# Kernel optimization log

Measured on AMD Instinct MI355X. Metric: run time of the kernel, lower is better.

Reference implementation:

```python
import jax, jax.numpy as jnp
import numpy as np

B, CIN, COUT, K, SDIM, H, W = 16, 512, 512, 3, 512, 64, 64


def setup_inputs() -> dict:
    key = jax.random.key(0)
    k1, k2, k3, k4 = jax.random.split(key, 4)
    return {
        "x": jax.random.normal(k1, (B, CIN, H, W), dtype=jnp.float32),
        "style": jax.random.normal(k2, (B, SDIM), dtype=jnp.float32),
        "weight": jax.random.normal(k3, (COUT, CIN, K, K), dtype=jnp.float32),
        "style_w": jax.random.normal(k4, (CIN, SDIM), dtype=jnp.float32),
        "style_b": jnp.ones((CIN,), dtype=jnp.float32),  # bias.data.fill_(1.0)
    }


def reference(x, style, weight, style_w, style_b):
    batch, in_ch, h, w_size = x.shape
    out_ch, _, ks, _ = weight.shape
    pad = ks // 2
    # EqualizedLinear: runtime weight scaling by 1/sqrt(fan_in)
    lin_scale = 1.0 / np.sqrt(style_w.shape[1])
    s = style @ (style_w * lin_scale).T + style_b  # [B, Cin]
    # modulate
    conv_scale = 1.0 / np.sqrt(in_ch * ks * ks)
    wmod = (weight[None] * conv_scale) * s[:, None, :, None, None]  # [B,Cout,Cin,k,k]
    # demodulate
    dcoef = jax.lax.rsqrt(jnp.sum(jnp.square(wmod), axis=(2, 3, 4)) + 1e-8)  # [B,Cout]
    wmod = wmod * dcoef[:, :, None, None, None]
    # grouped conv with groups = batch
    x_r = x.reshape(1, batch * in_ch, h, w_size)
    w_r = wmod.reshape(batch * out_ch, in_ch, ks, ks)
    out = jax.lax.conv_general_dilated(
        x_r, w_r,
        window_strides=(1, 1),
        padding=[(pad, pad), (pad, pad)],
        dimension_numbers=("NCHW", "OIHW", "NCHW"),
        feature_group_count=batch,
    )
    return out.reshape(batch, out_ch, h, w_size)
```

## Files before the change

kernel.cpp:

```cpp
#include <hip/hip_runtime.h>
#include <math.h>

#define B 16
#define CIN 512
#define COUT 512
#define SDIM 512
#define H 64
#define W 64

typedef short s16x8 __attribute__((ext_vector_type(8)));
typedef float f32x4 __attribute__((ext_vector_type(4)));
typedef float f32x16 __attribute__((ext_vector_type(16)));

__device__ __constant__ float LIN_SCALE  = 0.04419417382415922f;
__device__ __constant__ float CONV_SCALE = 0.014731391274719742f;

__device__ __forceinline__ ushort f2bf(float f) {
  unsigned u = __float_as_uint(f);
  return (ushort)((u + 0x7FFFu + ((u >> 16) & 1u)) >> 16);
}

#define GLOAD16(g, l)                                           \
  __builtin_amdgcn_global_load_lds(                             \
      (const __attribute__((address_space(1))) unsigned*)(g),   \
      (__attribute__((address_space(3))) unsigned*)(l), 16, 0, 0)

__global__ __launch_bounds__(512) void style_mod_kernel(
    const float* __restrict__ style, const float* __restrict__ style_w,
    const float* __restrict__ style_b, float* __restrict__ s,
    float* __restrict__ s2) {
  const int b = blockIdx.x;
  const int ci = threadIdx.x;
  __shared__ float st[SDIM];
  st[ci] = style[b * SDIM + ci];
  __syncthreads();

  const float4* wr = reinterpret_cast<const float4*>(style_w + (size_t)ci * SDIM);
  float acc = 0.f;
#pragma unroll 4
  for (int k = 0; k < SDIM / 4; ++k) {
    float4 wv = wr[k];
    acc += st[4 * k + 0] * wv.x + st[4 * k + 1] * wv.y +
           st[4 * k + 2] * wv.z + st[4 * k + 3] * wv.w;
  }
  float v = acc * LIN_SCALE + style_b[ci];
  s[b * CIN + ci] = v;
  s2[b * CIN + ci] = v * v;
}

__global__ __launch_bounds__(256) void wsq_kernel(
    const float* __restrict__ weight, float* __restrict__ wsq) {
  const int i = blockIdx.x * blockDim.x + threadIdx.x;
  if (i >= COUT * CIN) return;
  const float* p = weight + (size_t)i * 9;
  float a = 0.f;
#pragma unroll
  for (int k = 0; k < 9; ++k) {
    float v = p[k];
    a += v * v;
  }
  wsq[i] = a;
}

__global__ __launch_bounds__(512) void dcoef_kernel(
    const float* __restrict__ s2, const float* __restrict__ wsq,
    float* __restrict__ outscale) {
  const int b = blockIdx.x;
  const int co = threadIdx.x;
  __shared__ float sh[CIN];
  sh[co] = s2[b * CIN + co];
  __syncthreads();

  const float4* wr = reinterpret_cast<const float4*>(wsq + (size_t)co * CIN);
  float acc = 0.f;
#pragma unroll 4
  for (int k = 0; k < CIN / 4; ++k) {
    float4 wv = wr[k];
    acc += sh[4 * k + 0] * wv.x + sh[4 * k + 1] * wv.y +
           sh[4 * k + 2] * wv.z + sh[4 * k + 3] * wv.w;
  }
  float d = rsqrtf(acc * CONV_SCALE * CONV_SCALE + 1e-8f);
  outscale[b * COUT + co] = d * CONV_SCALE;
}

__global__ __launch_bounds__(256) void pack_w_kernel(
    const float* __restrict__ w, ushort* __restrict__ wt) {
  const int t = blockIdx.x * 256 + threadIdx.x;
  const int s = t & 3;
  const int chunk = (t >> 2) & 15;
  const int co = t >> 6;
  const float4* wp =
      (const float4*)(w + ((size_t)co * 512 + chunk * 32 + s * 8) * 9);
  float wv[72];
#pragma unroll
  for (int i = 0; i < 18; ++i) {
    float4 v = wp[i];
    wv[4 * i + 0] = v.x; wv[4 * i + 1] = v.y;
    wv[4 * i + 2] = v.z; wv[4 * i + 3] = v.w;
  }
  const int sp = s ^ ((co >> 1) & 3);
  ushort* dst = wt + (size_t)chunk * 147456 + (size_t)co * 32 + sp * 8;
#pragma unroll
  for (int j = 0; j < 9; ++j) {
    s16x8 p;
#pragma unroll
    for (int i = 0; i < 8; ++i) p[i] = (short)f2bf(wv[i * 9 + j]);
    *(s16x8*)(dst + (size_t)j * 16384) = p;
  }
}

__global__ __launch_bounds__(256) void pack_x_kernel(
    const float* __restrict__ x, const float* __restrict__ smod,
    ushort* __restrict__ xp) {
  __shared__ float xt[32][65];
  __shared__ float sm[32];
  const int tid = threadIdx.x;
  const int gr = blockIdx.x, chunk = blockIdx.y, b = blockIdx.z;
  if (tid < 32) sm[tid] = smod[b * 512 + chunk * 32 + tid];
  {
    const int ci = tid >> 3, cq = tid & 7;
    const float4* rp = (const float4*)(
        x + (((size_t)b * 512 + chunk * 32 + ci) * 64 + gr) * 64 + cq * 8);
    float4 a = rp[0], c2 = rp[1];
    float* row = &xt[ci][cq * 8];
    row[0] = a.x; row[1] = a.y; row[2] = a.z; row[3] = a.w;
    row[4] = c2.x; row[5] = c2.y; row[6] = c2.z; row[7] = c2.w;
  }
  __syncthreads();
  const int c = tid >> 2, s = tid & 3;
  s16x8 p;
#pragma unroll
  for (int i = 0; i < 8; ++i)
    p[i] = (short)f2bf(xt[s * 8 + i][c] * sm[s * 8 + i]);
  const int sp = s ^ (((c + 1) >> 1) & 3);
  *(s16x8*)(xp + ((size_t)(b * 16 + chunk) * 64 + gr) * 2048 + c * 32 + sp * 8) = p;
}

#define XS4OFF 36864
#define DLDS4 79104

__global__ __launch_bounds__(256, 2) void conv_mfma5_kernel(
    const ushort* __restrict__ wt, const ushort* __restrict__ xp,
    const float* __restrict__ outscale, float* __restrict__ out) {
  extern __shared__ char smem[];

  const int tid = threadIdx.x;
  const int hb = blockIdx.x;
  const int cb = blockIdx.y;
  const int b  = blockIdx.z;
  const int h0 = hb * 8, co0 = cb * 64;
  const int lane = tid & 63, wid = tid >> 6;
  const int l31 = lane & 31, hi = lane >> 5;

  {
    s16x8* p = (s16x8*)(smem + XS4OFF);
    for (int e = tid; e < 2640; e += 256) p[e] = (s16x8)0;
  }

  f32x16 acc[2][2][2];
#pragma unroll
  for (int rr = 0; rr < 2; ++rr)
#pragma unroll
    for (int mt = 0; mt < 2; ++mt)
#pragma unroll
      for (int nt = 0; nt < 2; ++nt) acc[rr][mt][nt] = (f32x16)0.f;

  const int akey = (l31 >> 1) & 3;
  int aoff[2][2];
#pragma unroll
  for (int mt = 0; mt < 2; ++mt)
#pragma unroll
    for (int ks = 0; ks < 2; ++ks)
      aoff[mt][ks] = (mt * 32 + l31) * 64 + ((ks * 2 + hi) ^ akey) * 16;

  int boff[3][2][2];
#pragma unroll
  for (int kw = 0; kw < 3; ++kw)
#pragma unroll
    for (int nt = 0; nt < 2; ++nt)
#pragma unroll
      for (int ks = 0; ks < 2; ++ks) {
        int cc = nt * 32 + l31 + kw;
        boff[kw][nt][ks] = cc * 64 + (((ks * 2 + hi) ^ ((cc >> 1) & 3))) * 16;
      }

  const char* wsrc0 = (const char*)wt + cb * 4096 + tid * 16;
  const char* xsrc0 = (const char*)xp + (size_t)b * 4194304 + tid * 16;
  char* wdst = smem + tid * 16;
  char* xdst = smem + XS4OFF + 64 + tid * 16;
  const char* wb = smem;
  const char* xb = smem + XS4OFF + 2 * wid * 4224;

  __syncthreads();

  for (int chunk = 0; chunk < 16; ++chunk) {
    const char* wsrc = wsrc0 + (size_t)chunk * 294912;
    const char* xsrc = xsrc0 + (size_t)chunk * 262144;
#pragma unroll
    for (int t = 0; t < 9; ++t)
      GLOAD16(wsrc + t * 32768, wdst + t * 4096);
#pragma unroll
    for (int t = 0; t < 10; ++t) {
      int gr = h0 - 1 + t;
      if ((unsigned)gr < 64u)
        GLOAD16(xsrc + (size_t)gr * 4096, xdst + t * 4224);
    }
    __syncthreads();

#pragma unroll
    for (int kw = 0; kw < 3; ++kw) {
      s16x8 bf[4][2][2];
#pragma unroll
      for (int q = 0; q < 4; ++q)
#pragma unroll
        for (int nt = 0; nt < 2; ++nt)
#pragma unroll
          for (int ks = 0; ks < 2; ++ks)
            bf[q][nt][ks] =
                *(const s16x8*)(xb + q * 4224 + boff[kw][nt][ks]);
#pragma unroll
      for (int kh = 0; kh < 3; ++kh) {
        const char* wj = wb + (kh * 3 + kw) * 4096;
#pragma unroll
        for (int ks = 0; ks < 2; ++ks) {
          s16x8 af0 = *(const s16x8*)(wj + aoff[0][ks]);
          s16x8 af1 = *(const s16x8*)(wj + aoff[1][ks]);
#pragma unroll
          for (int rr = 0; rr < 2; ++rr)
#pragma unroll
            for (int nt = 0; nt < 2; ++nt) {
              acc[rr][0][nt] = __builtin_amdgcn_mfma_f32_32x32x16_bf16(
                  af0, bf[rr + kh][nt][ks], acc[rr][0][nt], 0, 0, 0);
              acc[rr][1][nt] = __builtin_amdgcn_mfma_f32_32x32x16_bf16(
                  af1, bf[rr + kh][nt][ks], acc[rr][1][nt], 0, 0, 0);
            }
        }
      }
    }
    __syncthreads();
  }

#pragma unroll
  for (int mt = 0; mt < 2; ++mt) {
#pragma unroll
    for (int reg = 0; reg < 16; ++reg) {
      const int row = (reg & 3) + 8 * (reg >> 2) + 4 * hi;
      const int co = co0 + mt * 32 + row;
      const float osc = outscale[b * COUT + co];
      float* obase = out + ((size_t)b * COUT + co) * H * W;
#pragma unroll
      for (int rr = 0; rr < 2; ++rr) {
        const int h = h0 + 2 * wid + rr;
#pragma unroll
        for (int nt = 0; nt < 2; ++nt)
          obase[h * W + nt * 32 + l31] = acc[rr][mt][nt][reg] * osc;
      }
    }
  }
}

__global__ __launch_bounds__(256, 2) void conv_mfma2_kernel(
    const ushort* __restrict__ wt, const ushort* __restrict__ xp,
    const float* __restrict__ outscale, float* __restrict__ out) {
  __shared__ ushort ws[9][64][32];
  __shared__ ushort xs[6][66][32];

  const int tid = threadIdx.x;
  const int hb = blockIdx.x, cb = blockIdx.y, b = blockIdx.z;
  const int h0 = hb * 4, co0 = cb * 64;
  const int lane = tid & 63, wid = tid >> 6;
  const int l15 = lane & 15, l4 = lane >> 4;

  {
    s16x8* p = (s16x8*)&xs[0][0][0];
    for (int e = tid; e < 1584; e += 256) p[e] = (s16x8)0;
  }

  f32x4 acc[4][4];
#pragma unroll
  for (int mt = 0; mt < 4; ++mt)
#pragma unroll
    for (int nt = 0; nt < 4; ++nt) acc[mt][nt] = (f32x4)0.f;

  const int am = (l4 ^ ((l15 >> 1) & 3)) * 16;
  int aoff[4];
#pragma unroll
  for (int mt = 0; mt < 4; ++mt) aoff[mt] = (mt * 16 + l15) * 64 + am;
  int boff[12];
#pragma unroll
  for (int nt = 0; nt < 4; ++nt)
#pragma unroll
    for (int kw = 0; kw < 3; ++kw) {
      int col = nt * 16 + l15 + kw;
      boff[nt * 3 + kw] =
          wid * 4224 + col * 64 + ((l4 ^ ((col >> 1) & 3)) * 16);
    }

  const char* wsrc0 = (const char*)wt + cb * 4096 + wid * 1024 + lane * 16;
  const char* xsrc0 =
      (const char*)xp + (size_t)b * 4194304 + wid * 1024 + lane * 16;
  char* wdst = (char*)&ws[0][0][0] + wid * 1024 + lane * 16;
  char* xdst = (char*)&xs[0][0][0] + 64 + wid * 1024 + lane * 16;

  __syncthreads();

  for (int chunk = 0; chunk < 16; ++chunk) {
    const char* wsrc = wsrc0 + chunk * 294912;
    const char* xsrc = xsrc0 + chunk * 262144;
#pragma unroll
    for (int t = 0; t < 9; ++t)
      GLOAD16(wsrc + t * 32768, wdst + t * 4096);
#pragma unroll
    for (int t = 0; t < 6; ++t) {
      int gr = h0 - 1 + t;
      if ((unsigned)gr < 64u) GLOAD16(xsrc + gr * 4096, xdst + t * 4224);
    }
    __syncthreads();

#pragma unroll
    for (int kh = 0; kh < 3; ++kh) {
      const char* xrow = (const char*)&xs[0][0][0] + kh * 4224;
#pragma unroll
      for (int kw = 0; kw < 3; ++kw) {
        const int j = kh * 3 + kw;
        const char* wj = (const char*)&ws[0][0][0] + j * 4096;
        s16x8 af[4], bf[4];
#pragma unroll
        for (int mt = 0; mt < 4; ++mt)
          af[mt] = *(const s16x8*)(wj + aoff[mt]);
#pragma unroll
        for (int nt = 0; nt < 4; ++nt)
          bf[nt] = *(const s16x8*)(xrow + boff[nt * 3 + kw]);
#pragma unroll
        for (int mt = 0; mt < 4; ++mt)
#pragma unroll
          for (int nt = 0; nt < 4; ++nt)
            acc[mt][nt] = __builtin_amdgcn_mfma_f32_16x16x32_bf16(
                af[mt], bf[nt], acc[mt][nt], 0, 0, 0);
      }
    }
    __syncthreads();
  }

  const int h = h0 + wid;
#pragma unroll
  for (int mt = 0; mt < 4; ++mt) {
#pragma unroll
    for (int r = 0; r < 4; ++r) {
      const int co = co0 + mt * 16 + l4 * 4 + r;
      const float osc = outscale[b * COUT + co];
      float* orow = out + (((size_t)b * COUT + co) * H + h) * W;
#pragma unroll
      for (int nt = 0; nt < 4; ++nt)
        orow[nt * 16 + l15] = acc[mt][nt][r] * osc;
    }
  }
}

extern "C" void kernel_launch(void* const* d_in, const int* in_sizes, int n_in,
                              void* d_out, int out_size, void* d_ws,
                              size_t ws_size, hipStream_t stream) {
  const float* x = (const float*)d_in[0];
  const float* style = (const float*)d_in[1];
  const float* weight = (const float*)d_in[2];
  const float* style_w = (const float*)d_in[3];
  const float* style_b = (const float*)d_in[4];
  float* out = (float*)d_out;

  char* wsb = (char*)d_ws;
  float* s = (float*)(wsb + 0);
  float* s2 = (float*)(wsb + 32768);
  float* wsq = (float*)(wsb + 65536);
  float* outscale = (float*)(wsb + 1114112);
  ushort* wt = (ushort*)(wsb + 1146880);
  ushort* xp = (ushort*)(wsb + 5865472);
  const size_t NEED = 72974336;

  style_mod_kernel<<<B, 512, 0, stream>>>(style, style_w, style_b, s, s2);
  wsq_kernel<<<(COUT * CIN + 255) / 256, 256, 0, stream>>>(weight, wsq);
  dcoef_kernel<<<B, 512, 0, stream>>>(s2, wsq, outscale);

  pack_w_kernel<<<128, 256, 0, stream>>>(weight, wt);
  pack_x_kernel<<<dim3(64, 16, 16), 256, 0, stream>>>(x, s, xp);

  hipError_t attr_ok = hipFuncSetAttribute(
      reinterpret_cast<const void*>(conv_mfma5_kernel),
      hipFuncAttributeMaxDynamicSharedMemorySize, DLDS4);

  if (attr_ok == hipSuccess && ws_size >= NEED) {
    conv_mfma5_kernel<<<dim3(8, 8, 16), 256, DLDS4, stream>>>(wt, xp, outscale,
                                                              out);
  } else {
    conv_mfma2_kernel<<<dim3(16, 8, 16), 256, 0, stream>>>(wt, xp, outscale,
                                                           out);
  }
}
```

Baseline: 347.9 us.

## Fuse weight-square reduction into weight packing and use paired-column LDS swizzle

Removes the separate wsq kernel by computing per-(co,ci) sums of squared weights inside pack_w_kernel, which already loads those weights. Changes the packed bf16 layout for weights and activations so that two adjacent columns share a 128-byte row with an 8-way XOR swizzle, and updates the main MFMA kernel's fragment offsets to match. The aim is fewer LDS bank conflicts and one less pass over the weight tensor. The fallback path is replaced by a self-contained kernel that converts inputs in place; it does not run on the default path. The new swizzle has to agree exactly between the packers and the consumer.

Result: no change. 345.4 us (-0.7%).

```diff
diff --git a/kernel.cpp b/kernel.cpp
--- a/kernel.cpp
+++ b/kernel.cpp
@@ -18,6 +18,10 @@
 __device__ __forceinline__ ushort f2bf(float f) {
   unsigned u = __float_as_uint(f);
   return (ushort)((u + 0x7FFFu + ((u >> 16) & 1u)) >> 16);
+}
+
+__device__ __forceinline__ int slot_swz(int col, int o) {
+  return ((col & 1) * 4 + o) ^ ((col >> 1) & 7);
 }
 
 #define GLOAD16(g, l)                                           \
@@ -48,20 +52,6 @@
   s2[b * CIN + ci] = v * v;
 }
 
-__global__ __launch_bounds__(256) void wsq_kernel(
-    const float* __restrict__ weight, float* __restrict__ wsq) {
-  const int i = blockIdx.x * blockDim.x + threadIdx.x;
-  if (i >= COUT * CIN) return;
-  const float* p = weight + (size_t)i * 9;
-  float a = 0.f;
-#pragma unroll
-  for (int k = 0; k < 9; ++k) {
-    float v = p[k];
-    a += v * v;
-  }
-  wsq[i] = a;
-}
-
 __global__ __launch_bounds__(512) void dcoef_kernel(
     const float* __restrict__ s2, const float* __restrict__ wsq,
     float* __restrict__ outscale) {
@@ -84,7 +74,8 @@
 }
 
 __global__ __launch_bounds__(256) void pack_w_kernel(
-    const float* __restrict__ w, ushort* __restrict__ wt) {
+    const float* __restrict__ w, ushort* __restrict__ wt,
+    float* __restrict__ wsq) {
   const int t = blockIdx.x * 256 + threadIdx.x;
   const int s = t & 3;
   const int chunk = (t >> 2) & 15;
@@ -98,8 +89,24 @@
     wv[4 * i + 0] = v.x; wv[4 * i + 1] = v.y;
     wv[4 * i + 2] = v.z; wv[4 * i + 3] = v.w;
   }
-  const int sp = s ^ ((co >> 1) & 3);
-  ushort* dst = wt + (size_t)chunk * 147456 + (size_t)co * 32 + sp * 8;
+  {
+    float q[8];
+#pragma unroll
+    for (int i = 0; i < 8; ++i) {
+      float a = 0.f;
+#pragma unroll
+      for (int k = 0; k < 9; ++k) {
+        float v = wv[i * 9 + k];
+        a += v * v;
+      }
+      q[i] = a;
+    }
+    float4* qd = (float4*)(wsq + (size_t)co * 512 + chunk * 32 + s * 8);
+    qd[0] = make_float4(q[0], q[1], q[2], q[3]);
+    qd[1] = make_float4(q[4], q[5], q[6], q[7]);
+  }
+  const int sp = slot_swz(co, s);
+  ushort* dst = wt + (size_t)chunk * 147456 + (size_t)(co >> 1) * 64 + sp * 8;
 #pragma unroll
   for (int j = 0; j < 9; ++j) {
     s16x8 p;
@@ -127,19 +134,20 @@
     row[4] = c2.x; row[5] = c2.y; row[6] = c2.z; row[7] = c2.w;
   }
   __syncthreads();
-  const int c = tid >> 2, s = tid & 3;
+  const int c = tid >> 2, o = tid & 3;
   s16x8 p;
 #pragma unroll
   for (int i = 0; i < 8; ++i)
-    p[i] = (short)f2bf(xt[s * 8 + i][c] * sm[s * 8 + i]);
-  const int sp = s ^ (((c + 1) >> 1) & 3);
-  *(s16x8*)(xp + ((size_t)(b * 16 + chunk) * 64 + gr) * 2048 + c * 32 + sp * 8) = p;
+    p[i] = (short)f2bf(xt[o * 8 + i][c] * sm[o * 8 + i]);
+  const int cc = c + 1;
+  const int off_us = (cc >> 1) * 64 + slot_swz(cc, o) * 8 - 32;
+  *(s16x8*)(xp + ((size_t)(b * 16 + chunk) * 64 + gr) * 2048 + off_us) = p;
 }
 
 #define XS4OFF 36864
 #define DLDS4 79104
 
-__global__ __launch_bounds__(256, 2) void conv_mfma5_kernel(
+__global__ __launch_bounds__(256, 2) void conv_mfma6_kernel(
     const ushort* __restrict__ wt, const ushort* __restrict__ xp,
     const float* __restrict__ outscale, float* __restrict__ out) {
   extern __shared__ char smem[];
@@ -165,14 +173,14 @@
 #pragma unroll
       for (int nt = 0; nt < 2; ++nt) acc[rr][mt][nt] = (f32x16)0.f;
 
-  const int akey = (l31 >> 1) & 3;
   int aoff[2][2];
 #pragma unroll
   for (int mt = 0; mt < 2; ++mt)
 #pragma unroll
-    for (int ks = 0; ks < 2; ++ks)
-      aoff[mt][ks] = (mt * 32 + l31) * 64 + ((ks * 2 + hi) ^ akey) * 16;
-
+    for (int ks = 0; ks < 2; ++ks) {
+      int co = mt * 32 + l31;
+      aoff[mt][ks] = (co >> 1) * 128 + slot_swz(co, ks * 2 + hi) * 16;
+    }
   int boff[3][2][2];
 #pragma unroll
   for (int kw = 0; kw < 3; ++kw)
@@ -181,7 +189,7 @@
 #pragma unroll
       for (int ks = 0; ks < 2; ++ks) {
         int cc = nt * 32 + l31 + kw;
-        boff[kw][nt][ks] = cc * 64 + (((ks * 2 + hi) ^ ((cc >> 1) & 3))) * 16;
+        boff[kw][nt][ks] = (cc >> 1) * 128 + slot_swz(cc, ks * 2 + hi) * 16;
       }
 
   const char* wsrc0 = (const char*)wt + cb * 4096 + tid * 16;
@@ -259,22 +267,23 @@
   }
 }
 
-__global__ __launch_bounds__(256, 2) void conv_mfma2_kernel(
-    const ushort* __restrict__ wt, const ushort* __restrict__ xp,
-    const float* __restrict__ outscale, float* __restrict__ out) {
+__global__ __launch_bounds__(256, 2) void conv_mfma_kernel(
+    const float* __restrict__ x, const float* __restrict__ weight,
+    const float* __restrict__ s, const float* __restrict__ outscale,
+    float* __restrict__ out) {
+  __shared__ ushort xs[6][66][32];
   __shared__ ushort ws[9][64][32];
-  __shared__ ushort xs[6][66][32];
 
   const int tid = threadIdx.x;
-  const int hb = blockIdx.x, cb = blockIdx.y, b = blockIdx.z;
-  const int h0 = hb * 4, co0 = cb * 64;
-  const int lane = tid & 63, wid = tid >> 6;
-  const int l15 = lane & 15, l4 = lane >> 4;
-
-  {
-    s16x8* p = (s16x8*)&xs[0][0][0];
-    for (int e = tid; e < 1584; e += 256) p[e] = (s16x8)0;
-  }
+  const int hb = blockIdx.x;
+  const int cb = blockIdx.y;
+  const int b  = blockIdx.z;
+  const int h0 = hb * 4;
+  const int co0 = cb * 64;
+  const int lane = tid & 63;
+  const int wid = tid >> 6;
+  const int l15 = lane & 15;
+  const int l4  = lane >> 4;
 
   f32x4 acc[4][4];
 #pragma unroll
@@ -282,55 +291,71 @@
 #pragma unroll
     for (int nt = 0; nt < 4; ++nt) acc[mt][nt] = (f32x4)0.f;
 
-  const int am = (l4 ^ ((l15 >> 1) & 3)) * 16;
-  int aoff[4];
-#pragma unroll
-  for (int mt = 0; mt < 4; ++mt) aoff[mt] = (mt * 16 + l15) * 64 + am;
-  int boff[12];
-#pragma unroll
-  for (int nt = 0; nt < 4; ++nt)
-#pragma unroll
-    for (int kw = 0; kw < 3; ++kw) {
-      int col = nt * 16 + l15 + kw;
-      boff[nt * 3 + kw] =
-          wid * 4224 + col * 64 + ((l4 ^ ((col >> 1) & 3)) * 16);
-    }
-
-  const char* wsrc0 = (const char*)wt + cb * 4096 + wid * 1024 + lane * 16;
-  const char* xsrc0 =
-      (const char*)xp + (size_t)b * 4194304 + wid * 1024 + lane * 16;
-  char* wdst = (char*)&ws[0][0][0] + wid * 1024 + lane * 16;
-  char* xdst = (char*)&xs[0][0][0] + 64 + wid * 1024 + lane * 16;
-
-  __syncthreads();
-
-  for (int chunk = 0; chunk < 16; ++chunk) {
-    const char* wsrc = wsrc0 + chunk * 294912;
-    const char* xsrc = xsrc0 + chunk * 262144;
-#pragma unroll
-    for (int t = 0; t < 9; ++t)
-      GLOAD16(wsrc + t * 32768, wdst + t * 4096);
-#pragma unroll
-    for (int t = 0; t < 6; ++t) {
-      int gr = h0 - 1 + t;
-      if ((unsigned)gr < 64u) GLOAD16(xsrc + gr * 4096, xdst + t * 4224);
+  const int wq = tid & 3;
+  const int wco = tid >> 2;
+
+  for (int c0 = 0; c0 < CIN; c0 += 32) {
+    {
+      const float4* wp = reinterpret_cast<const float4*>(
+          weight + ((size_t)(co0 + wco) * CIN + c0 + wq * 8) * 9);
+      float wv[72];
+#pragma unroll
+      for (int t = 0; t < 18; ++t) {
+        float4 v = wp[t];
+        wv[4 * t + 0] = v.x; wv[4 * t + 1] = v.y;
+        wv[4 * t + 2] = v.z; wv[4 * t + 3] = v.w;
+      }
+      float sv[8];
+#pragma unroll
+      for (int i = 0; i < 8; ++i) sv[i] = s[b * CIN + c0 + wq * 8 + i];
+#pragma unroll
+      for (int j = 0; j < 9; ++j) {
+        s16x8 p;
+#pragma unroll
+        for (int i = 0; i < 8; ++i)
+          p[i] = (short)f2bf(wv[i * 9 + j] * sv[i]);
+        *reinterpret_cast<s16x8*>(&ws[j][wco][wq * 8]) = p;
+      }
+    }
+#pragma unroll
+    for (int it = 0; it < 7; ++it) {
+      int e = tid + it * 256;
+      if (e < 6 * 66 * 4) {
+        int q = e & 3;
+        int t2 = e >> 2;
+        int cc = t2 % 66;
+        int r = t2 / 66;
+        int gr = h0 - 1 + r;
+        int gc = cc - 1;
+        s16x8 p;
+        if ((unsigned)gr < H && (unsigned)gc < W) {
+          const float* xp2 =
+              x + (((size_t)b * CIN + c0 + q * 8) * H + gr) * W + gc;
+#pragma unroll
+          for (int i = 0; i < 8; ++i) p[i] = (short)f2bf(xp2[(size_t)i * H * W]);
+        } else {
+#pragma unroll
+          for (int i = 0; i < 8; ++i) p[i] = 0;
+        }
+        *reinterpret_cast<s16x8*>(&xs[r][cc][q * 8]) = p;
+      }
     }
     __syncthreads();
 
 #pragma unroll
     for (int kh = 0; kh < 3; ++kh) {
-      const char* xrow = (const char*)&xs[0][0][0] + kh * 4224;
 #pragma unroll
       for (int kw = 0; kw < 3; ++kw) {
         const int j = kh * 3 + kw;
-        const char* wj = (const char*)&ws[0][0][0] + j * 4096;
         s16x8 af[4], bf[4];
 #pragma unroll
         for (int mt = 0; mt < 4; ++mt)
-          af[mt] = *(const s16x8*)(wj + aoff[mt]);
+          af[mt] = *reinterpret_cast<const s16x8*>(
+              &ws[j][mt * 16 + l15][l4 * 8]);
 #pragma unroll
         for (int nt = 0; nt < 4; ++nt)
-          bf[nt] = *(const s16x8*)(xrow + boff[nt * 3 + kw]);
+          bf[nt] = *reinterpret_cast<const s16x8*>(
+              &xs[wid + kh][nt * 16 + l15 + kw][l4 * 8]);
 #pragma unroll
         for (int mt = 0; mt < 4; ++mt)
 #pragma unroll
@@ -376,22 +401,20 @@
   ushort* xp = (ushort*)(wsb + 5865472);
   const size_t NEED = 72974336;
 
+  hipError_t attr_ok = hipFuncSetAttribute(
+      reinterpret_cast<const void*>(conv_mfma6_kernel),
+      hipFuncAttributeMaxDynamicSharedMemorySize, DLDS4);
+
   style_mod_kernel<<<B, 512, 0, stream>>>(style, style_w, style_b, s, s2);
-  wsq_kernel<<<(COUT * CIN + 255) / 256, 256, 0, stream>>>(weight, wsq);
+  pack_w_kernel<<<128, 256, 0, stream>>>(weight, wt, wsq);
   dcoef_kernel<<<B, 512, 0, stream>>>(s2, wsq, outscale);
 
-  pack_w_kernel<<<128, 256, 0, stream>>>(weight, wt);
-  pack_x_kernel<<<dim3(64, 16, 16), 256, 0, stream>>>(x, s, xp);
-
-  hipError_t attr_ok = hipFuncSetAttribute(
-      reinterpret_cast<const void*>(conv_mfma5_kernel),
-      hipFuncAttributeMaxDynamicSharedMemorySize, DLDS4);
-
   if (attr_ok == hipSuccess && ws_size >= NEED) {
-    conv_mfma5_kernel<<<dim3(8, 8, 16), 256, DLDS4, stream>>>(wt, xp, outscale,
+    pack_x_kernel<<<dim3(64, 16, 16), 256, 0, stream>>>(x, s, xp);
+    conv_mfma6_kernel<<<dim3(8, 8, 16), 256, DLDS4, stream>>>(wt, xp, outscale,
                                                               out);
   } else {
-    conv_mfma2_kernel<<<dim3(16, 8, 16), 256, 0, stream>>>(wt, xp, outscale,
-                                                           out);
-  }
-}
+    conv_mfma_kernel<<<dim3(16, 8, 16), 256, 0, stream>>>(x, weight, s,
+                                                          outscale, out);
+  }
+}
```
